# Kernel tuning notes

Hardware: AMD Instinct MI355X
Metric: run time of the kernel (lower is better)

The kernel has to match this reference:

```python
import jax, jax.numpy as jnp
import numpy as np

B, N, C, HF, WF = 32, 1000, 64, 12, 20
Y_DISC = 72
D = C * HF  # 768: flattened anchor feature dim (channels x fv height)


def setup_inputs() -> dict:
    key = jax.random.key(0)
    ks = jax.random.split(key, 8)
    feature_volumes = jax.random.normal(ks[0], (B, C, HF, WF), jnp.float32)
    # Anchor gather indices: channel index, row index, per-anchor x along the anchor line
    z_idx = jnp.broadcast_to(jnp.arange(C, dtype=jnp.int32)[None, :, None], (N, C, HF))
    y_idx = jnp.broadcast_to(jnp.arange(HF, dtype=jnp.int32)[None, None, :], (N, C, HF))
    x_line = jax.random.randint(ks[1], (N, 1, HF), 0, WF, dtype=jnp.int32)
    x_idx = jnp.broadcast_to(x_line, (N, C, HF))
    invalid_mask = jnp.broadcast_to(jax.random.bernoulli(ks[2], 0.2, (N, 1, HF)), (N, C, HF))
    attn_w = jax.random.normal(ks[3], (D, N - 1), jnp.float32) * 0.02
    attn_b = jnp.zeros((N - 1,), jnp.float32)
    cls_w = jax.random.normal(ks[4], (2 * D, 2), jnp.float32) * 0.02
    cls_b = jnp.zeros((2,), jnp.float32)
    reg_w = jax.random.normal(ks[5], (2 * D, Y_DISC + 1), jnp.float32) * 0.02
    reg_b = jnp.zeros((Y_DISC + 1,), jnp.float32)
    anchors_image = jax.random.normal(ks[6], (N, 5 + Y_DISC), jnp.float32)
    return {
        'feature_volumes': feature_volumes,
        'attn_w': attn_w, 'attn_b': attn_b,
        'cls_w': cls_w, 'cls_b': cls_b,
        'reg_w': reg_w, 'reg_b': reg_b,
        'anchors_image': anchors_image,
        'z_idx': z_idx, 'y_idx': y_idx, 'x_idx': x_idx,
        'invalid_mask': invalid_mask,
    }


def reference(feature_volumes, attn_w, attn_b, cls_w, cls_b, reg_w, reg_b,
              anchors_image, z_idx, y_idx, x_idx, invalid_mask):
    b = feature_volumes.shape[0]
    n = z_idx.shape[0]
    # __cut_anchor_features: gather (B, N, C, HF) rois, zero invalid entries
    rois = feature_volumes[:, z_idx, y_idx, x_idx]          # (B, N, C, HF)
    rois = jnp.where(invalid_mask[None], 0.0, rois)
    feat = rois.reshape(b, n, D)                            # (B, N, D)
    # attention layer: Linear(D -> N-1) + softmax over the N-1 dim
    scores = jax.nn.softmax(feat @ attn_w + attn_b, axis=-1)  # (B, N, N-1)
    # scatter scores into the off-diagonal of an NxN matrix (diagonal = 0)
    rows = jnp.arange(n)
    k = jnp.arange(n - 1)
    col_idx = jnp.where(k[None, :] < rows[:, None], k[None, :], k[None, :] + 1)  # (N, N-1)
    attn_mat = jnp.zeros((b, n, n), feat.dtype).at[:, rows[:, None], col_idx].set(scores)
    # bmm: attention-weighted sum of anchor features
    att_feat = jnp.einsum('bij,bjd->bid', attn_mat, feat)   # (B, N, D)
    cat = jnp.concatenate([att_feat, feat], axis=-1)        # (B, N, 2D)
    cls_logits = cat @ cls_w + cls_b                        # (B, N, 2)
    reg = cat @ reg_w + reg_b                               # (B, N, 73)
    anchors = jnp.broadcast_to(anchors_image[None], (b, n, 5 + Y_DISC))
    # proposals: [:2]=cls, [2:4]=anchor, [4:]=anchor+reg
    return jnp.concatenate([cls_logits, anchors[:, :, 2:4], anchors[:, :, 4:] + reg], axis=-1)
```

## Files before the change

kernel.cpp:

```cpp
#include <hip/hip_runtime.h>
#include <hip/hip_bf16.h>

typedef _Float16 f16;
typedef _Float16 f16x4 __attribute__((ext_vector_type(4)));
typedef _Float16 f16x8 __attribute__((ext_vector_type(8)));
typedef float    f32x4 __attribute__((ext_vector_type(4)));

static __device__ __forceinline__ float bf2f(__hip_bfloat16 x) { return __bfloat162float(x); }
static __device__ __forceinline__ float ldf(const void* p, long i, int f32flag) {
    return f32flag ? ((const float*)p)[i] : bf2f(((const __hip_bfloat16*)p)[i]);
}
static __device__ __forceinline__ void stf(void* p, long i, int f32flag, float v) {
    if (f32flag) ((float*)p)[i] = v;
    else ((__hip_bfloat16*)p)[i] = __float2bfloat16(v);
}
static __device__ __forceinline__ void gl2lds16(const f16* g, f16* l) {
    __builtin_amdgcn_global_load_lds(
        (const __attribute__((address_space(1))) unsigned int*)(const void*)g,
        (__attribute__((address_space(3))) unsigned int*)(void*)l, 16, 0, 0);
}

#define OFF_LOGITS 0L
#define SZ_LOGITS  (32000L * 1024 * 2)
#define OFF_FEAT   (OFF_LOGITS + SZ_LOGITS)
#define SZ_FEAT    (32000L * 768 * 2)
#define OFF_F12    (OFF_FEAT + SZ_FEAT)
#define SZ_F12     (32000L * 256 * 2)
#define OFF_AWT    (OFF_F12 + SZ_F12)
#define SZ_AWT     (1024L * 768 * 2)
#define OFF_WCT    (OFF_AWT + SZ_AWT)
#define SZ_WCT     (256L * 768 * 2)
#define OFF_BIAS   (OFF_WCT + SZ_WCT)
#define OFF_AB     (OFF_BIAS + 512)
#define OFF_FLAG   (OFF_AB + 4096)
#define OFF_F1T    (OFF_FLAG + 64)
#define SZ_F1T     (32L * 128 * 1024 * 2)
#define NEED_A     (OFF_F1T + SZ_F1T)

__global__ void detect_kernel(const unsigned int* __restrict__ fv,
                              const unsigned int* __restrict__ m,
                              int mwords, int* __restrict__ flags)
{
    __shared__ int cnt, bits;
    int t = threadIdx.x;
    if (t == 0) { cnt = 0; bits = 0; }
    __syncthreads();
    int c = 0;
    for (int k = t; k < 2048; k += 256) {
        unsigned int w = fv[k];
        unsigned int h0 = w & 0xffffu, h1 = w >> 16;
        unsigned int e0 = (h0 >> 7) & 0xffu, e1 = (h1 >> 7) & 0xffu;
        c += (h0 == 0u || (e0 >= 100u && e0 <= 135u)) ? 1 : 0;
        c += (h1 == 0u || (e1 >= 100u && e1 <= 135u)) ? 1 : 0;
    }
    atomicAdd(&cnt, c);
    int lb = 0;
    for (int k = t; k < mwords; k += 256) {
        unsigned int w = m[k];
        if (w > 1u) lb |= 1;
        if ((k & 1) && w != 0u) lb |= 2;
        unsigned int lo = w & 0xffffu, hi = w >> 16;
        if (!((lo == 0u || lo == 0x3f80u) && (hi == 0u || hi == 0x3f80u))) lb |= 4;
        if (lo == 0x3f80u) lb |= 8;
    }
    if (lb) atomicOr(&bits, lb);
    __syncthreads();
    if (t == 0) {
        int b = bits, f;
        if (!(b & 1))      f = (b & 2) ? 0 : 3;
        else if (!(b & 4)) f = (b & 8) ? 2 : 4;
        else               f = 1;
        flags[0] = f;
        flags[1] = (cnt < 3900) ? 1 : 0;
    }
}

__global__ __launch_bounds__(256) void front_kernel(
    const void* __restrict__ fv, const int* __restrict__ x_idx,
    const void* __restrict__ maskp, const int* __restrict__ flags,
    int xstride, int mstride, f16* __restrict__ feat,
    const void* __restrict__ attn_w,
    const void* __restrict__ cls_w, const void* __restrict__ cls_b,
    const void* __restrict__ reg_w, const void* __restrict__ reg_b,
    const void* __restrict__ attn_b,
    f16* __restrict__ awT, f16* __restrict__ wcT,
    float* __restrict__ biasc, float* __restrict__ abf32)
{
    int bid = blockIdx.x;
    int t = threadIdx.x;
    int isf = flags[1], fm = flags[0];
    if (bid < 512) {
        __shared__ f16 sfv[15360];
        __shared__ int sx[756];
        __shared__ unsigned char sm[756];
        int b = bid >> 4, n0 = (bid & 15) * 63;
        int rows = min(63, 1000 - n0);
        if (isf) {
            const float4* src = (const float4*)fv + (long)b * 3840;
            for (int k = t; k < 3840; k += 256) {
                float4 v = src[k];
                f16x4 h; h[0] = (f16)v.x; h[1] = (f16)v.y; h[2] = (f16)v.z; h[3] = (f16)v.w;
                *(f16x4*)&sfv[k * 4] = h;
            }
        } else {
            const uint4* src = (const uint4*)fv + (long)b * 1920;
            for (int k = t; k < 1920; k += 256) {
                uint4 v = src[k];
                unsigned int wv[4] = {v.x, v.y, v.z, v.w};
                f16x8 h;
                #pragma unroll
                for (int j = 0; j < 4; j++) {
                    h[2 * j]     = (f16)__uint_as_float((wv[j] & 0xffffu) << 16);
                    h[2 * j + 1] = (f16)__uint_as_float(wv[j] & 0xffff0000u);
                }
                *(f16x8*)&sfv[k * 8] = h;
            }
        }
        for (int k = t; k < rows * 12; k += 256) {
            int n = k / 12, h = k - n * 12;
            sx[k] = x_idx[(long)(n0 + n) * xstride + h];
            long mb = (long)(n0 + n) * mstride + h;
            int mv;
            if (fm == 0)      mv = ((const int*)maskp)[mb] != 0;
            else if (fm == 1) mv = ((const unsigned char*)maskp)[mb] != 0;
            else if (fm == 2) mv = ((const unsigned short*)maskp)[mb] != 0;
            else if (fm == 3) mv = ((const int*)maskp)[mb * 2] != 0;
            else              mv = ((const unsigned int*)maskp)[mb] != 0;
            sm[k] = (unsigned char)mv;
        }
        __syncthreads();
        for (int q = t; q < rows * 192; q += 256) {
            int n = q / 192, r = q - n * 192;
            int e0 = r * 4;
            f16x4 v;
            #pragma unroll
            for (int j = 0; j < 4; j++) {
                int e = e0 + j;
                int h = e % 12;
                int kk = n * 12 + h;
                v[j] = sm[kk] ? (f16)0.f : sfv[e * 20 + sx[kk]];
            }
            *(f16x4*)(feat + ((long)(b * 1000 + n0 + n)) * 768 + e0) = v;
        }
    } else if (bid < 1280) {
        __shared__ f16 tile[32][33];
        int tid = bid - 512;
        int c0 = (tid % 32) * 32, r0 = (tid / 32) * 32;
        int tx = t & 31, ty = t >> 5;
        #pragma unroll
        for (int i = ty; i < 32; i += 8) {
            int r = r0 + i, c = c0 + tx;
            float v = 0.f;
            if (r < 768 && c < 999) v = ldf(attn_w, (long)r * 999 + c, isf);
            tile[i][tx] = (f16)v;
        }
        __syncthreads();
        #pragma unroll
        for (int i = ty; i < 32; i += 8) {
            int oc = c0 + i, orw = r0 + tx;
            awT[(long)oc * 768 + orw] = tile[tx][i];
        }
    } else {
        int idx = (bid - 1280) * 256 + t;
        if (idx < 256 * 768) {
            int c = idx / 768, k = idx - c * 768;
            int wrow = (c < 128) ? k : 768 + k;
            int wcol = (c < 128) ? c : c - 128;
            float v = 0.f;
            if (wcol < 2)       v = ldf(cls_w, (long)wrow * 2 + wcol, isf);
            else if (wcol < 75) v = ldf(reg_w, (long)wrow * 73 + (wcol - 2), isf);
            wcT[idx] = (f16)v;
        }
        if (idx < 75)
            biasc[idx] = (idx < 2) ? ldf(cls_b, idx, isf) : ldf(reg_b, idx - 2, isf);
        if (idx < 1024)
            abf32[idx] = (idx < 999) ? ldf(attn_b, idx, isf) : 0.f;
    }
}

__global__ __launch_bounds__(256) void post_kernel(
    f16* __restrict__ buf, const float* __restrict__ abf32,
    const f16* __restrict__ F12, f16* __restrict__ F1T)
{
    int bid = blockIdx.x;
    int t = threadIdx.x;
    if (bid < 1024) {
        __shared__ f16 tile[64][68];
        int bz = bid >> 5;
        int rq = bid & 31;
        int by = rq & 15, bx = rq >> 4;
        int r0 = by * 64, c0 = bx * 64;
        int tr = t >> 4, tc = (t & 15) * 4;
        const f16* src = F12 + (long)bz * 1000 * 256;
        #pragma unroll
        for (int ii = 0; ii < 4; ii++) {
            int r = r0 + ii * 16 + tr;
            f16x4 v = {(f16)0.f, (f16)0.f, (f16)0.f, (f16)0.f};
            if (r < 1000) v = *(const f16x4*)(src + (long)r * 256 + c0 + tc);
            *(f16x4*)&tile[ii * 16 + tr][tc] = v;
        }
        __syncthreads();
        f16* dst = F1T + (long)bz * 131072;
        #pragma unroll
        for (int ii = 0; ii < 4; ii++) {
            int d = ii * 16 + tr;
            f16x4 v;
            #pragma unroll
            for (int j = 0; j < 4; j++) v[j] = tile[tc + j][d];
            *(f16x4*)(dst + (long)(c0 + d) * 1024 + r0 + tc) = v;
        }
        return;
    }
    int rid = bid - 1024;
    int i = rid % 1000, b = rid / 1000;
    f16* row = buf + ((long)(b * 1000 + i)) * 1024;
    __shared__ float red[8];
    __shared__ float epv[256];
    int k0 = t * 4;
    f16x4 rv = *(const f16x4*)(row + k0);
    float4 ab = *(const float4*)(abf32 + k0);
    float abv[4] = {ab.x, ab.y, ab.z, ab.w};
    float v[4];
    float lmax = -3.4e38f;
    #pragma unroll
    for (int j = 0; j < 4; j++) {
        int k = k0 + j;
        float x = (k < 999) ? (float)rv[j] + abv[j] : -3.4e38f;
        v[j] = x;
        lmax = fmaxf(lmax, x);
    }
    #pragma unroll
    for (int o = 32; o > 0; o >>= 1) lmax = fmaxf(lmax, __shfl_down(lmax, o, 64));
    if ((t & 63) == 0) red[t >> 6] = lmax;
    __syncthreads();
    float gmax = fmaxf(fmaxf(red[0], red[1]), fmaxf(red[2], red[3]));
    float e[4];
    float lsum = 0.f;
    #pragma unroll
    for (int j = 0; j < 4; j++) {
        int k = k0 + j;
        float x = (k < 999) ? __expf(v[j] - gmax) : 0.f;
        e[j] = x;
        lsum += x;
    }
    epv[t] = e[3];
    #pragma unroll
    for (int o = 32; o > 0; o >>= 1) lsum += __shfl_down(lsum, o, 64);
    if ((t & 63) == 0) red[4 + (t >> 6)] = lsum;
    __syncthreads();
    float inv = 1.f / (red[4] + red[5] + red[6] + red[7]);
    f16x4 outv;
    if (k0 >= 1000) {
        #pragma unroll
        for (int j = 0; j < 4; j++) outv[j] = (f16)0.f;
    } else if (k0 + 3 < i) {
        #pragma unroll
        for (int j = 0; j < 4; j++) outv[j] = (f16)(e[j] * inv);
    } else if (k0 > i) {
        float ep = epv[t - 1];
        outv[0] = (f16)(ep * inv);
        #pragma unroll
        for (int j = 1; j < 4; j++) outv[j] = (f16)(e[j - 1] * inv);
    } else {
        #pragma unroll
        for (int j = 0; j < 4; j++) {
            int p = k0 + j;
            float s = (p == i) ? 0.f : ((p < i) ? e[j] : e[j - 1 < 0 ? 0 : j - 1]);
            if (p > i) s = e[j - 1];
            outv[j] = (f16)(s * inv);
        }
    }
    *(f16x4*)(row + k0) = outv;
}

#define SB8   __builtin_amdgcn_sched_barrier(0)
#define BAR8  __builtin_amdgcn_s_barrier()
#define LGKM0 do { asm volatile("s_waitcnt lgkmcnt(0)" ::: "memory"); __builtin_amdgcn_sched_barrier(0); } while (0)
#define VM4   asm volatile("s_waitcnt vmcnt(4)" ::: "memory")

__global__ __launch_bounds__(512, 2) void gemm8p_kernel(
    const f16* __restrict__ A, int lda,
    const f16* __restrict__ Bt, int ldb,
    f16* __restrict__ C, int ldc,
    int M, int MT, int NT, int KT,
    long sA, long sB, long sC)
{
    __shared__ __align__(16) f16 As[2][16384];
    __shared__ __align__(16) f16 Bs[2][16384];
    int t = threadIdx.x;
    int nwg = gridDim.x;
    int orig = blockIdx.x;
    int xcd = orig & 7, lin = orig >> 3;
    int q8 = nwg >> 3, r8 = nwg & 7;
    int wgid = (xcd < r8 ? xcd * (q8 + 1) : r8 * (q8 + 1) + (xcd - r8) * q8) + lin;
    int per_b = MT * NT;
    int bz = wgid / per_b;
    int rem = wgid - bz * per_b;
    int mt = rem / NT, nt = rem - mt * NT;
    int m0 = mt * 256, n0 = nt * 256;
    A  += (long)bz * sA;
    Bt += (long)bz * sB;
    C  += (long)bz * sC;
    int w = t >> 6, lane = t & 63;
    int wm = (w >> 2) * 128, wn = (w & 3) * 64;
    int lr = lane & 15, lq = lane >> 4;
    int row0 = t >> 3, slot = t & 7;
    int csw = slot ^ (row0 & 7);

    f32x4 acc[8][4];
    const f32x4 z4 = {0.f, 0.f, 0.f, 0.f};
    #pragma unroll
    for (int i = 0; i < 8; i++)
        #pragma unroll
        for (int j = 0; j < 4; j++) acc[i][j] = z4;

    f16x8 a_[2][2], b_[4][2];

#define STAGE_A8(kt, h, buf) do { \
    int ktc = (kt) < KT ? (kt) : KT - 1; \
    const f16* gp = A + (long)(m0 + (h) * 128 + row0) * lda + ktc * 64 + csw * 8; \
    gl2lds16(gp,                  &As[buf][(h) * 8192 + w * 512]); \
    gl2lds16(gp + 64 * (long)lda, &As[buf][(h) * 8192 + 4096 + w * 512]); \
} while (0)
#define STAGE_B8(kt, h, buf) do { \
    int ktc = (kt) < KT ? (kt) : KT - 1; \
    const f16* gp = Bt + (long)(n0 + (h) * 128 + row0) * ldb + ktc * 64 + csw * 8; \
    gl2lds16(gp,                  &Bs[buf][(h) * 8192 + w * 512]); \
    gl2lds16(gp + 64 * (long)ldb, &Bs[buf][(h) * 8192 + 4096 + w * 512]); \
} while (0)
#define RD_B8(buf) { \
    _Pragma("unroll") for (int n = 0; n < 4; n++) { \
        int r = wn + n * 16 + lr; int rb = r * 64; int x7 = r & 7; \
        _Pragma("unroll") for (int ks = 0; ks < 2; ks++) { \
            int cc = (lq + ks * 4) ^ x7; \
            b_[n][ks] = *(const f16x8*)&Bs[buf][rb + cc * 8]; } } }
#define RD_A8(q, buf) { \
    _Pragma("unroll") for (int m2 = 0; m2 < 2; m2++) { \
        int r = wm + ((q) * 2 + m2) * 16 + lr; int rb = r * 64; int x7 = r & 7; \
        _Pragma("unroll") for (int ks = 0; ks < 2; ks++) { \
            int cc = (lq + ks * 4) ^ x7; \
            a_[m2][ks] = *(const f16x8*)&As[buf][rb + cc * 8]; } } }
#define MFMA16(q) { \
    __builtin_amdgcn_s_setprio(1); \
    _Pragma("unroll") for (int ks = 0; ks < 2; ks++) \
    _Pragma("unroll") for (int m2 = 0; m2 < 2; m2++) \
    _Pragma("unroll") for (int n = 0; n < 4; n++) \
        acc[(q) * 2 + m2][n] = __builtin_amdgcn_mfma_f32_16x16x32_f16( \
            a_[m2][ks], b_[n][ks], acc[(q) * 2 + m2][n], 0, 0, 0); \
    __builtin_amdgcn_s_setprio(0); }

    STAGE_B8(0, 0, 0); STAGE_B8(0, 1, 0);
    STAGE_A8(0, 0, 0); STAGE_A8(0, 1, 0);
    STAGE_B8(1, 0, 1); STAGE_B8(1, 1, 1);
    VM4;
    BAR8;

    int NIT = KT >> 1;
    for (int it = 0; it < NIT; it++) {
        int t0 = 2 * it, t1 = t0 + 1;
        SB8; RD_B8(0); RD_A8(0, 0); STAGE_A8(t1, 0, 1);
        BAR8; LGKM0; MFMA16(0); BAR8;
        SB8; RD_A8(1, 0); STAGE_A8(t1, 1, 1);
        BAR8; LGKM0; MFMA16(1); BAR8;
        SB8; RD_A8(2, 0); STAGE_B8(t0 + 2, 0, 0);
        BAR8; LGKM0; MFMA16(2); BAR8;
        SB8; RD_A8(3, 0); STAGE_B8(t0 + 2, 1, 0);
        BAR8; LGKM0; MFMA16(3); VM4; BAR8;
        SB8; RD_B8(1); RD_A8(0, 1); STAGE_A8(t0 + 2, 0, 0);
        BAR8; LGKM0; MFMA16(0); BAR8;
        SB8; RD_A8(1, 1); STAGE_A8(t0 + 2, 1, 0);
        BAR8; LGKM0; MFMA16(1); BAR8;
        SB8; RD_A8(2, 1); STAGE_B8(t1 + 2, 0, 1);
        BAR8; LGKM0; MFMA16(2); BAR8;
        SB8; RD_A8(3, 1); STAGE_B8(t1 + 2, 1, 1);
        BAR8; LGKM0; MFMA16(3); VM4; BAR8;
    }

    #pragma unroll
    for (int m = 0; m < 8; m++)
        #pragma unroll
        for (int n = 0; n < 4; n++)
            #pragma unroll
            for (int r = 0; r < 4; r++) {
                int gm = m0 + wm + m * 16 + lq * 4 + r;
                int gn = n0 + wn + n * 16 + lr;
                if (gm < M) C[(long)gm * ldc + gn] = (f16)acc[m][n][r];
            }
#undef STAGE_A8
#undef STAGE_B8
#undef RD_B8
#undef RD_A8
#undef MFMA16
}

enum { OUT_F16 = 0, OUT_FINAL = 1 };

template<int MODE, bool CAT, bool BKM, int TM, int TN, int BK, int SWZ, bool BG>
__global__ __launch_bounds__(256, 2) void gemm_kernel(
    const f16* __restrict__ A, const f16* __restrict__ A2, int lda,
    const f16* __restrict__ Bt, int ldb,
    void* __restrict__ Cout, int ldc,
    int M, int Nc, int K,
    long sA, long sB, long sC,
    const float* __restrict__ bias, const void* __restrict__ anchors,
    const int* __restrict__ flags, const f16* __restrict__ F2c)
{
    int t = threadIdx.x;
    int bx, by, bz;
    bx = blockIdx.x; by = blockIdx.y; bz = blockIdx.z;

    int m0 = by * TM, n0 = bx * TN;
    int z = bz;
    A  += (long)z * sA;
    if (CAT) A2 += (long)z * sA;
    Bt += (long)z * sB;
    int w = t >> 6, lane = t & 63;
    constexpr int NJ = (TM == 128 && TN == 256) ? 8 : ((TN == 256) ? 4 : ((TM == 128) ? 4 : 2));
    int wm = (TM == 128) ? (w & 1) * 64 : 0;
    int wn;
    if constexpr (TM == 128 && TN == 256) wn = (w >> 1) * 128;
    else if constexpr (TN == 256)         wn = w * 64;
    else if constexpr (TM == 128)         wn = (w >> 1) * 64;
    else                                  wn = w * 32;

    int lr = lane & 15, lq = lane >> 4;

    const f32x4 zero4 = {0.f, 0.f, 0.f, 0.f};
    f32x4 acc[4][NJ];
    #pragma unroll
    for (int i = 0; i < 4; i++)
        #pragma unroll
        for (int j = 0; j < NJ; j++) acc[i][j] = zero4;

    if constexpr (BG) {
        constexpr int CH  = BK / 8;
        constexpr int AI  = TM * BK / 2048;
        constexpr int RPO = 2048 / BK;
        __shared__ __align__(16) f16 As[TM * BK];
        int row0 = t / CH, slot = t % CH;
        int csw = slot ^ (row0 & (CH - 1));
        long aoffB = (long)(m0 + row0) * lda + csw * 8;
        for (int k0 = 0; k0 < K; k0 += BK) {
            const f16* Ak = A; int kk = k0;
            if (CAT && k0 >= 768) { Ak = A2; kk = k0 - 768; }
            __syncthreads();
            #pragma unroll
            for (int i = 0; i < AI; i++)
                gl2lds16(Ak + aoffB + (long)(i * RPO) * lda + kk, &As[i * 2048 + w * 512]);
            f16x8 ball[BK / 32][NJ];
            #pragma unroll
            for (int ks = 0; ks < BK / 32; ks++)
                #pragma unroll
                for (int j = 0; j < NJ; j++) {
                    int r = wn + j * 16 + lr;
                    ball[ks][j] = *(const f16x8*)(Bt + (long)(n0 + r) * ldb + k0 + (ks * 4 + lq) * 8);
                }
            __syncthreads();
            #pragma unroll
            for (int ks = 0; ks < BK / 32; ks++) {
                f16x8 af[4];
                #pragma unroll
                for (int i = 0; i < 4; i++) {
                    int r = wm + i * 16 + lr;
                    int cc = (lq + ks * 4) ^ (r & (CH - 1));
                    af[i] = *(const f16x8*)&As[r * BK + cc * 8];
                }
                #pragma unroll
                for (int i = 0; i < 4; i++)
                    #pragma unroll
                    for (int j = 0; j < NJ; j++)
                        acc[i][j] = __builtin_amdgcn_mfma_f32_16x16x32_f16(af[i], ball[ks][j], acc[i][j], 0, 0, 0);
            }
        }
    } else {
        constexpr int CH  = BK / 8;
        constexpr int AI  = TM * BK / 2048;
        constexpr int BI  = TN * BK / 2048;
        constexpr int RPO = 2048 / BK;
        __shared__ __align__(16) f16 As[TM * BK];
        __shared__ __align__(16) f16 Bs[TN * BK];
        int row0 = t / CH, slot = t % CH;
        int csw = slot ^ (row0 & (CH - 1));
        long aoffB = (long)(m0 + row0) * lda + csw * 8;
        long boffB = (long)(n0 + row0) * ldb + csw * 8;
        for (int k0 = 0; k0 < K; k0 += BK) {
            const f16* Ak = A; int kk = k0;
            if (CAT && k0 >= 768) { Ak = A2; kk = k0 - 768; }
            __syncthreads();
            #pragma unroll
            for (int i = 0; i < AI; i++)
                gl2lds16(Ak + aoffB + (long)(i * RPO) * lda + kk, &As[i * 2048 + w * 512]);
            #pragma unroll
            for (int i = 0; i < BI; i++)
                gl2lds16(Bt + boffB + (long)(i * RPO) * ldb + k0, &Bs[i * 2048 + w * 512]);
            __syncthreads();
            #pragma unroll
            for (int ks = 0; ks < BK / 32; ks++) {
                f16x8 af[4], bfr[NJ];
                #pragma unroll
                for (int i = 0; i < 4; i++) {
                    int r = wm + i * 16 + lr;
                    int cc = (lq + ks * 4) ^ (r & (CH - 1));
                    af[i] = *(const f16x8*)&As[r * BK + cc * 8];
                }
                #pragma unroll
                for (int j = 0; j < NJ; j++) {
                    int r = wn + j * 16 + lr;
                    int cc = (lq + ks * 4) ^ (r & (CH - 1));
                    bfr[j] = *(const f16x8*)&Bs[r * BK + cc * 8];
                }
                #pragma unroll
                for (int i = 0; i < 4; i++)
                    #pragma unroll
                    for (int j = 0; j < NJ; j++)
                        acc[i][j] = __builtin_amdgcn_mfma_f32_16x16x32_f16(af[i], bfr[j], acc[i][j], 0, 0, 0);
            }
        }
    }

    int isf = (MODE == OUT_FINAL) ? flags[1] : 0;
    #pragma unroll
    for (int i = 0; i < 4; i++) {
        #pragma unroll
        for (int j = 0; j < NJ; j++) {
            #pragma unroll
            for (int r = 0; r < 4; r++) {
                int gm = m0 + wm + i * 16 + lq * 4 + r;
                int gn = n0 + wn + j * 16 + lr;
                if (MODE == OUT_F16) {
                    if (gm < M && gn < Nc)
                        ((f16*)Cout)[(long)z * sC + (long)gm * ldc + gn] = (f16)acc[i][j][r];
                } else {
                    if (gm < M) {
                        if (gn < Nc) {
                            float v = acc[i][j][r] + bias[gn];
                            if (F2c) v += (float)F2c[((long)z * 1000 + gm) * 256 + 128 + gn];
                            int oc = (gn < 2) ? gn : gn + 2;
                            if (gn >= 2) v += ldf(anchors, (long)(gm % 1000) * 77 + oc, isf);
                            stf(Cout, (long)z * sC + (long)gm * 77 + oc, isf, v);
                        } else if (gn < 77) {
                            int oc = gn - 73;
                            stf(Cout, (long)z * sC + (long)gm * 77 + oc, isf,
                                ldf(anchors, (long)(gm % 1000) * 77 + oc, isf));
                        }
                    }
                }
            }
        }
    }
}

extern "C" void kernel_launch(void* const* d_in, const int* in_sizes, int n_in,
                              void* d_out, int out_size, void* d_ws, size_t ws_size,
                              hipStream_t stream)
{
    const void* fv      = d_in[0];
    const void* attn_w  = d_in[1];
    const void* attn_b  = d_in[2];
    const void* cls_w   = d_in[3];
    const void* cls_b   = d_in[4];
    const void* reg_w   = d_in[5];
    const void* reg_b   = d_in[6];
    const void* anchors = d_in[7];
    const int*  x_idx   = (const int*)d_in[10];
    const void* maskp   = d_in[11];
    int xstride = (in_sizes[10] < 768000) ? 12 : 768;
    int mstride = (in_sizes[11] < 768000) ? 12 : 768;
    int mwords  = in_sizes[11] / 4;
    if (mwords > 4096) mwords = 4096;

    char* ws = (char*)d_ws;
    f16*   logits = (f16*)(ws + OFF_LOGITS);
    f16*   feat   = (f16*)(ws + OFF_FEAT);
    f16*   F12    = (f16*)(ws + OFF_F12);
    f16*   awT    = (f16*)(ws + OFF_AWT);
    f16*   wcT2   = (f16*)(ws + OFF_WCT);
    float* biasc  = (float*)(ws + OFF_BIAS);
    float* abf32  = (float*)(ws + OFF_AB);
    int*   flags  = (int*)(ws + OFF_FLAG);
    f16*   F1T    = (f16*)(ws + OFF_F1T);

    detect_kernel<<<dim3(1), dim3(256), 0, stream>>>(
        (const unsigned int*)fv, (const unsigned int*)maskp, mwords, flags);
    front_kernel<<<dim3(2048), dim3(256), 0, stream>>>(
        fv, x_idx, maskp, flags, xstride, mstride, feat,
        attn_w, cls_w, cls_b, reg_w, reg_b, attn_b, awT, wcT2, biasc, abf32);

    gemm_kernel<OUT_F16, false, false, 64, 128, 128, 0, true><<<dim3(2, 500, 1), dim3(256), 0, stream>>>(
        feat, nullptr, 768, wcT2, 768, F12, 256, 32000, 256, 768, 0, 0, 0,
        nullptr, nullptr, flags, nullptr);

    gemm8p_kernel<<<dim3(500), dim3(512), 0, stream>>>(
        feat, 768, awT, 768, logits, 1024, 32000, 125, 4, 12, 0L, 0L, 0L);
    post_kernel<<<dim3(1024 + 32000), dim3(256), 0, stream>>>(logits, abf32, F12, F1T);

    gemm_kernel<OUT_FINAL, false, false, 64, 128, 128, 0, true><<<dim3(1, 16, 32), dim3(256), 0, stream>>>(
        logits, nullptr, 1024, F1T, 1024, d_out, 77, 1000, 75, 1024,
        1024000L, 131072L, 77000L, biasc, anchors, flags, F12);
}
```

Baseline: 294.3 us.

## Load B operand directly from global in big GEMM, drop B LDS staging

Removes the shared-memory buffers and async staging for the B (attention weight) operand in the 256x256 GEMM, so each wave reads its B fragments straight from global memory (the weights stay cache-resident). This halves LDS use, and launch bounds are raised to 4 waves-per-EU hints to allow more occupancy. The wait on outstanding loads changes from vmcnt(4) to vmcnt(0), which serializes more: the direct global B loads now sit on the critical path before the MFMAs, with no prefetch overlap.

Result: slower. 617.1 us (+109.7%).

```diff
diff --git a/kernel.cpp b/kernel.cpp
--- a/kernel.cpp
+++ b/kernel.cpp
@@ -276,9 +276,9 @@
 #define SB8   __builtin_amdgcn_sched_barrier(0)
 #define BAR8  __builtin_amdgcn_s_barrier()
 #define LGKM0 do { asm volatile("s_waitcnt lgkmcnt(0)" ::: "memory"); __builtin_amdgcn_sched_barrier(0); } while (0)
-#define VM4   asm volatile("s_waitcnt vmcnt(4)" ::: "memory")
-
-__global__ __launch_bounds__(512, 2) void gemm8p_kernel(
+#define VM0   asm volatile("s_waitcnt vmcnt(0)" ::: "memory")
+
+__global__ __launch_bounds__(512, 4) void gemm8pbg_kernel(
     const f16* __restrict__ A, int lda,
     const f16* __restrict__ Bt, int ldb,
     f16* __restrict__ C, int ldc,
@@ -286,7 +286,6 @@
     long sA, long sB, long sC)
 {
     __shared__ __align__(16) f16 As[2][16384];
-    __shared__ __align__(16) f16 Bs[2][16384];
     int t = threadIdx.x;
     int nwg = gridDim.x;
     int orig = blockIdx.x;
@@ -322,18 +321,11 @@
     gl2lds16(gp,                  &As[buf][(h) * 8192 + w * 512]); \
     gl2lds16(gp + 64 * (long)lda, &As[buf][(h) * 8192 + 4096 + w * 512]); \
 } while (0)
-#define STAGE_B8(kt, h, buf) do { \
-    int ktc = (kt) < KT ? (kt) : KT - 1; \
-    const f16* gp = Bt + (long)(n0 + (h) * 128 + row0) * ldb + ktc * 64 + csw * 8; \
-    gl2lds16(gp,                  &Bs[buf][(h) * 8192 + w * 512]); \
-    gl2lds16(gp + 64 * (long)ldb, &Bs[buf][(h) * 8192 + 4096 + w * 512]); \
-} while (0)
-#define RD_B8(buf) { \
+#define RD_BG(kt) { \
     _Pragma("unroll") for (int n = 0; n < 4; n++) { \
-        int r = wn + n * 16 + lr; int rb = r * 64; int x7 = r & 7; \
-        _Pragma("unroll") for (int ks = 0; ks < 2; ks++) { \
-            int cc = (lq + ks * 4) ^ x7; \
-            b_[n][ks] = *(const f16x8*)&Bs[buf][rb + cc * 8]; } } }
+        long rb = (long)(n0 + wn + n * 16 + lr) * ldb + (kt) * 64; \
+        _Pragma("unroll") for (int ks = 0; ks < 2; ks++) \
+            b_[n][ks] = *(const f16x8*)(Bt + rb + (lq + ks * 4) * 8); } }
 #define RD_A8(q, buf) { \
     _Pragma("unroll") for (int m2 = 0; m2 < 2; m2++) { \
         int r = wm + ((q) * 2 + m2) * 16 + lr; int rb = r * 64; int x7 = r & 7; \
@@ -349,31 +341,29 @@
             a_[m2][ks], b_[n][ks], acc[(q) * 2 + m2][n], 0, 0, 0); \
     __builtin_amdgcn_s_setprio(0); }
 
-    STAGE_B8(0, 0, 0); STAGE_B8(0, 1, 0);
     STAGE_A8(0, 0, 0); STAGE_A8(0, 1, 0);
-    STAGE_B8(1, 0, 1); STAGE_B8(1, 1, 1);
-    VM4;
+    VM0;
     BAR8;
 
     int NIT = KT >> 1;
     for (int it = 0; it < NIT; it++) {
         int t0 = 2 * it, t1 = t0 + 1;
-        SB8; RD_B8(0); RD_A8(0, 0); STAGE_A8(t1, 0, 1);
+        SB8; RD_BG(t0); RD_A8(0, 0); STAGE_A8(t1, 0, 1);
         BAR8; LGKM0; MFMA16(0); BAR8;
         SB8; RD_A8(1, 0); STAGE_A8(t1, 1, 1);
         BAR8; LGKM0; MFMA16(1); BAR8;
-        SB8; RD_A8(2, 0); STAGE_B8(t0 + 2, 0, 0);
+        SB8; RD_A8(2, 0);
         BAR8; LGKM0; MFMA16(2); BAR8;
-        SB8; RD_A8(3, 0); STAGE_B8(t0 + 2, 1, 0);
-        BAR8; LGKM0; MFMA16(3); VM4; BAR8;
-        SB8; RD_B8(1); RD_A8(0, 1); STAGE_A8(t0 + 2, 0, 0);
+        SB8; RD_A8(3, 0);
+        BAR8; LGKM0; MFMA16(3); VM0; BAR8;
+        SB8; RD_BG(t1); RD_A8(0, 1); STAGE_A8(t0 + 2, 0, 0);
         BAR8; LGKM0; MFMA16(0); BAR8;
         SB8; RD_A8(1, 1); STAGE_A8(t0 + 2, 1, 0);
         BAR8; LGKM0; MFMA16(1); BAR8;
-        SB8; RD_A8(2, 1); STAGE_B8(t1 + 2, 0, 1);
+        SB8; RD_A8(2, 1);
         BAR8; LGKM0; MFMA16(2); BAR8;
-        SB8; RD_A8(3, 1); STAGE_B8(t1 + 2, 1, 1);
-        BAR8; LGKM0; MFMA16(3); VM4; BAR8;
+        SB8; RD_A8(3, 1);
+        BAR8; LGKM0; MFMA16(3); VM0; BAR8;
     }
 
     #pragma unroll
@@ -387,8 +377,7 @@
                 if (gm < M) C[(long)gm * ldc + gn] = (f16)acc[m][n][r];
             }
 #undef STAGE_A8
-#undef STAGE_B8
-#undef RD_B8
+#undef RD_BG
 #undef RD_A8
 #undef MFMA16
 }
@@ -590,7 +579,7 @@
         feat, nullptr, 768, wcT2, 768, F12, 256, 32000, 256, 768, 0, 0, 0,
         nullptr, nullptr, flags, nullptr);
 
-    gemm8p_kernel<<<dim3(500), dim3(512), 0, stream>>>(
+    gemm8pbg_kernel<<<dim3(500), dim3(512), 0, stream>>>(
         feat, 768, awT, 768, logits, 1024, 32000, 125, 4, 12, 0L, 0L, 0L);
     post_kernel<<<dim3(1024 + 32000), dim3(256), 0, stream>>>(logits, abf32, F12, F1T);
 
```
